# Kernel optimization log

Hardware: AMD Instinct MI355X
Metric: run time of the kernel (lower is better)

The kernel has to match this reference:

```python
import jax, jax.numpy as jnp
import numpy as np

N_NODES = 100000
N_EDGES = 1600000
D = 128  # feat_input_size_node == embed_inside_size == feat_target_size


def gcn_layer(x, W, b, row, col, ew, n_nodes):
    """PyG GCNConv with scalar edge_weight, add_self_loops=True, normalize=True.
    x: [N, Fin], W: [Fout, Fin], b: [Fout], row/col: [E], ew: [E].
    Messages flow row -> col (source_to_target)."""
    h = x @ W.T  # [N, Fout]
    # degree includes self-loop weight 1.0 per node
    deg = jax.ops.segment_sum(ew, col, num_segments=n_nodes) + 1.0  # [N]
    dinv = jnp.where(deg > 0, jax.lax.rsqrt(deg), 0.0)  # [N]
    norm = dinv[row] * ew * dinv[col]  # [E]
    msgs = norm[:, None] * h[row]  # [E, Fout] -- gather
    agg = jax.ops.segment_sum(msgs, col, num_segments=n_nodes)  # scatter-add
    agg = agg + (dinv * dinv)[:, None] * h  # self-loop contribution (weight 1)
    return agg + b


def setup_inputs() -> dict:
    key = jax.random.key(0)
    k1, k2, k3, k4, k5, k6, k7 = jax.random.split(key, 7)
    edge_tuples = jax.random.randint(k1, (2, N_EDGES), 0, N_NODES, dtype=jnp.int64) if jax.config.jax_enable_x64 else jax.random.randint(k1, (2, N_EDGES), 0, N_NODES).astype(jnp.int32)
    edge_feats = jax.random.uniform(k2, (N_EDGES, 1), dtype=jnp.float32)
    node_feats = jax.random.normal(k3, (N_NODES, D), dtype=jnp.float32)
    s1 = 1.0 / np.sqrt(D)
    W1 = jax.random.uniform(k4, (D, D), minval=-s1, maxval=s1, dtype=jnp.float32)
    b1 = jnp.zeros((D,), dtype=jnp.float32)
    W2 = jax.random.uniform(k5, (D, D), minval=-s1, maxval=s1, dtype=jnp.float32)
    b2 = jnp.zeros((D,), dtype=jnp.float32)
    return {"edge_tuples": edge_tuples, "edge_feats": edge_feats, "node_feats": node_feats,
            "W1": W1, "b1": b1, "W2": W2, "b2": b2}


def reference(edge_tuples, edge_feats, node_feats, W1, b1, W2, b2):
    row, col = edge_tuples[0], edge_tuples[1]
    ew = edge_feats.squeeze(-1)  # [E]
    n = node_feats.shape[0]
    h = gcn_layer(node_feats, W1, b1, row, col, ew, n)
    h = jnp.tanh(h)  # activate='tanh' between the two GCN layers
    out = gcn_layer(h, W2, b2, row, col, ew, n)
    # skip=Identity (Fin==Fout), doskip=1
    return out + node_feats
```

## Files before the change

### kernel.cpp

```cpp
#include <hip/hip_runtime.h>
#include <math.h>

#define D 128
#define SCAN_T 256
#define EPB 4096
#define MAXNB 800

typedef unsigned long long ull;
typedef unsigned short ushort_t;
typedef __attribute__((ext_vector_type(8))) short bf16x8;
typedef __attribute__((ext_vector_type(4))) float f32x4;

__device__ __forceinline__ float bf_lo(unsigned u) { return __uint_as_float(u << 16); }
__device__ __forceinline__ float bf_hi(unsigned u) { return __uint_as_float(u & 0xffff0000u); }
__device__ __forceinline__ unsigned bpack(float a, float b) {
  unsigned ua = __float_as_uint(a), ub = __float_as_uint(b);
  ua += 0x7fff + ((ua >> 16) & 1);
  ub += 0x7fff + ((ub >> 16) & 1);
  return (ua >> 16) | (ub & 0xffff0000u);
}
__device__ __forceinline__ ushort_t bh16(float a) {
  unsigned ua = __float_as_uint(a);
  ua += 0x7fff + ((ua >> 16) & 1);
  return (ushort_t)(ua >> 16);
}

__global__ __launch_bounds__(256) void k_h1(const int* __restrict__ col, int E, int B1, int B1pad,
                                            int* __restrict__ gh, int NB,
                                            const float2* __restrict__ x2, unsigned* __restrict__ xb, int n64,
                                            const float* __restrict__ W1, const float* __restrict__ W2,
                                            ushort_t* __restrict__ Whi1, ushort_t* __restrict__ Wlo1,
                                            ushort_t* __restrict__ Whi2, ushort_t* __restrict__ Wlo2) {
  int b = blockIdx.x, t = threadIdx.x;
  if (b < B1) {
    __shared__ int h[MAXNB];
    for (int i = t; i < NB; i += 256) h[i] = 0;
    __syncthreads();
    int e0 = b * EPB, e1 = min(E, e0 + EPB);
    for (int e = e0 + t; e < e1; e += 256) atomicAdd(&h[col[e] >> 7], 1);
    __syncthreads();
    for (int i = t; i < NB; i += 256) gh[i * B1pad + b] = h[i];
    return;
  }
  int idx = (b - B1) * 256 + t;
  if (idx < n64) { float2 v = x2[idx]; xb[idx] = bpack(v.x, v.y); return; }
  int j = idx - n64;
  if (j >= 2 * D * D) return;
  const float* W = (j < D * D) ? W1 : W2;
  ushort_t* Hh = (j < D * D) ? Whi1 : Whi2;
  ushort_t* Hl = (j < D * D) ? Wlo1 : Wlo2;
  int k = j & (D * D - 1);
  float w = W[k];
  ushort_t hh = bh16(w);
  Hh[k] = hh;
  Hl[k] = bh16(w - __uint_as_float((unsigned)hh << 16));
}

__global__ __launch_bounds__(512) void k_hscan(int* __restrict__ gh, int* __restrict__ binTotal,
                                               int B1, int B1pad) {
  __shared__ int wsum[8];
  int bin = blockIdx.x, t = threadIdx.x;
  int v = (t < B1) ? gh[bin * B1pad + t] : 0;
  int lane = t & 63, wid = t >> 6;
  int x = v;
  #pragma unroll
  for (int d = 1; d < 64; d <<= 1) { int y = __shfl_up(x, d, 64); if (lane >= d) x += y; }
  if (lane == 63) wsum[wid] = x;
  __syncthreads();
  int woff = 0;
  for (int w = 0; w < wid; ++w) woff += wsum[w];
  if (t < B1) gh[bin * B1pad + t] = woff + x - v;
  if (t == 511) binTotal[bin] = woff + x;
}

__device__ __forceinline__ int block_excl_scan(int v, int t, int* wsum, int* total) {
  int lane = t & 63, wid = t >> 6;
  int x = v;
  #pragma unroll
  for (int d = 1; d < 64; d <<= 1) {
    int y = __shfl_up(x, d, 64);
    if (lane >= d) x += y;
  }
  if (lane == 63) wsum[wid] = x;
  __syncthreads();
  int woff = 0;
  for (int w = 0; w < wid; ++w) woff += wsum[w];
  if (total) { int tot = 0; for (int w = 0; w < 4; ++w) tot += wsum[w]; *total = tot; }
  return woff + x - v;
}

__global__ __launch_bounds__(SCAN_T) void k_hscan2(const int* __restrict__ binTotal,
                                                   int* __restrict__ binBase,
                                                   int* __restrict__ offs, int NB, int N) {
  __shared__ int wsum[4];
  int t = threadIdx.x;
  int base = t * 4;
  int v[4]; int s = 0;
  #pragma unroll
  for (int u = 0; u < 4; ++u) { v[u] = (base + u < NB) ? binTotal[base + u] : 0; s += v[u]; }
  int tot;
  int excl = block_excl_scan(s, t, wsum, &tot);
  int run = excl;
  #pragma unroll
  for (int u = 0; u < 4; ++u) { if (base + u < NB) binBase[base + u] = run; run += v[u]; }
  if (t == 0) { binBase[NB] = tot; offs[N] = tot; }
}

__global__ __launch_bounds__(256) void k_scatter(const int* __restrict__ row, const int* __restrict__ col,
                                                 const float* __restrict__ ew,
                                                 const int* __restrict__ gh, const int* __restrict__ binBase,
                                                 int B1pad, int NB,
                                                 ull* __restrict__ a_e, int E) {
  __shared__ ull recs[EPB];
  __shared__ int hist[MAXNB];
  __shared__ int cur[MAXNB];
  __shared__ int wb[MAXNB];
  __shared__ int wsum[4];
  int b = blockIdx.x, t = threadIdx.x;
  for (int i = t; i < NB; i += 256) { hist[i] = 0; cur[i] = 0; }
  __syncthreads();
  int e0 = b * EPB;
  int cnt = min(E - e0, EPB);
  ull v[16];
  #pragma unroll
  for (int k = 0; k < 16; ++k) {
    int idx = t + k * 256;
    v[k] = 0;
    if (idx < cnt) {
      int e = e0 + idx;
      int c = col[e];
      unsigned q = __float2uint_rn(ew[e] * 32767.0f);
      if (q > 32767u) q = 32767u;
      unsigned hi = ((unsigned)c << 15) | q;
      v[k] = ((ull)hi << 32) | (unsigned)row[e];
      atomicAdd(&hist[hi >> 22], 1);
    }
  }
  __syncthreads();
  int base = t * 4;
  int hv[4];
  #pragma unroll
  for (int u = 0; u < 4; ++u) hv[u] = (base + u < NB) ? hist[base + u] : 0;
  int s = hv[0] + hv[1] + hv[2] + hv[3];
  int excl = block_excl_scan(s, t, wsum, nullptr);
  int run = excl;
  #pragma unroll
  for (int u = 0; u < 4; ++u) {
    if (base + u < NB) {
      hist[base + u] = run;
      wb[base + u] = binBase[base + u] + gh[(base + u) * B1pad + b] - run;
    }
    run += hv[u];
  }
  __syncthreads();
  #pragma unroll
  for (int k = 0; k < 16; ++k) {
    if (t + k * 256 < cnt) {
      unsigned bkt = (unsigned)(v[k] >> 54);
      int idx = hist[bkt] + atomicAdd(&cur[bkt], 1);
      recs[idx] = v[k];
    }
  }
  __syncthreads();
  for (int i = t; i < cnt; i += 256) {
    ull r = recs[i];
    a_e[wb[(unsigned)(r >> 54)] + i] = r;
  }
}

__global__ __launch_bounds__(256) void k_bucket(const ull* __restrict__ a_e,
                                                const int* __restrict__ binBase,
                                                int* __restrict__ offs, float* __restrict__ dinv,
                                                unsigned* __restrict__ sorted2, int N) {
  __shared__ int hist[128];
  __shared__ float wdeg[128];
  __shared__ int pfx[128];
  __shared__ int cur[128];
  int bin = blockIdx.x, t = threadIdx.x;
  if (t < 128) { hist[t] = 0; wdeg[t] = 0.f; cur[t] = 0; }
  __syncthreads();
  int s0 = binBase[bin], s1 = binBase[bin + 1];
  for (int i = s0 + t; i < s1; i += 256) {
    unsigned hi = (unsigned)(a_e[i] >> 32);
    int lc = (hi >> 15) & 127;
    atomicAdd(&hist[lc], 1);
    atomicAdd(&wdeg[lc], (float)(hi & 32767u) * (1.0f / 32767.0f));
  }
  __syncthreads();
  if (t == 0) { int run = 0; for (int i = 0; i < 128; ++i) { pfx[i] = run; run += hist[i]; } }
  __syncthreads();
  int c0 = bin << 7;
  if (t < 128 && c0 + t < N) {
    offs[c0 + t] = s0 + pfx[t];
    dinv[c0 + t] = rsqrtf(wdeg[t] + 1.0f);
  }
  for (int i = s0 + t; i < s1; i += 256) {
    ull v = a_e[i];
    unsigned hi = (unsigned)(v >> 32);
    int lc = (hi >> 15) & 127;
    int pos = s0 + pfx[lc] + atomicAdd(&cur[lc], 1);
    sorted2[pos] = ((unsigned)v << 15) | (hi & 32767u);
  }
}

__global__ void k_norm(unsigned* __restrict__ el, const int* __restrict__ offs,
                       const float* __restrict__ dinv, int N) {
  int c = blockIdx.x * blockDim.x + threadIdx.x;
  if (c >= N) return;
  int s0 = offs[c], s1 = offs[c + 1];
  float dc = dinv[c] * (1.0f / 32767.0f);
  for (int i = s0; i < s1; ++i) {
    unsigned v = el[i];
    unsigned r = v >> 15;
    float nrm = dinv[r] * (float)(v & 32767u) * dc;
    unsigned q = __float2uint_rn(nrm * 32767.0f);
    if (q > 32767u) q = 32767u;
    el[i] = (r << 15) | q;
  }
}

__global__ __launch_bounds__(256) void k_agg(const unsigned* __restrict__ H2,
                                             const unsigned* __restrict__ elist,
                                             const int* __restrict__ offs, const float* __restrict__ dinv,
                                             unsigned* __restrict__ outb, int N) {
  int lane = threadIdx.x & 63;
  int c = blockIdx.x * 4 + (threadIdx.x >> 6);
  if (c >= N) return;
  int start = offs[c];
  int m = offs[c + 1] - start;
  int q = lane >> 4;
  int fi = lane & 15;
  float a0 = 0.f, a1 = 0.f, a2 = 0.f, a3 = 0.f, a4 = 0.f, a5 = 0.f, a6 = 0.f, a7 = 0.f;
  for (int base = 0; base < m; base += 64) {
    int chunk = min(64, m - base);
    unsigned rec = (lane < chunk) ? elist[start + base + lane] : 0u;
    int iters = (chunk + 3) >> 2;
    int i = 0;
    for (; i + 4 <= iters; i += 4) {
      unsigned e0 = __shfl(rec, 4 * i + q, 64);
      unsigned e1 = __shfl(rec, 4 * i + 4 + q, 64);
      unsigned e2 = __shfl(rec, 4 * i + 8 + q, 64);
      unsigned e3 = __shfl(rec, 4 * i + 12 + q, 64);
      uint4 u0 = *(const uint4*)&H2[(size_t)(e0 >> 15) * 64 + fi * 4];
      uint4 u1 = *(const uint4*)&H2[(size_t)(e1 >> 15) * 64 + fi * 4];
      uint4 u2 = *(const uint4*)&H2[(size_t)(e2 >> 15) * 64 + fi * 4];
      uint4 u3 = *(const uint4*)&H2[(size_t)(e3 >> 15) * 64 + fi * 4];
      float w0 = (float)(e0 & 0x7fffu) * (1.0f / 32767.0f);
      float w1 = (float)(e1 & 0x7fffu) * (1.0f / 32767.0f);
      float w2 = (float)(e2 & 0x7fffu) * (1.0f / 32767.0f);
      float w3 = (float)(e3 & 0x7fffu) * (1.0f / 32767.0f);
      a0 += w0 * bf_lo(u0.x); a1 += w0 * bf_hi(u0.x);
      a2 += w0 * bf_lo(u0.y); a3 += w0 * bf_hi(u0.y);
      a4 += w0 * bf_lo(u0.z); a5 += w0 * bf_hi(u0.z);
      a6 += w0 * bf_lo(u0.w); a7 += w0 * bf_hi(u0.w);
      a0 += w1 * bf_lo(u1.x); a1 += w1 * bf_hi(u1.x);
      a2 += w1 * bf_lo(u1.y); a3 += w1 * bf_hi(u1.y);
      a4 += w1 * bf_lo(u1.z); a5 += w1 * bf_hi(u1.z);
      a6 += w1 * bf_lo(u1.w); a7 += w1 * bf_hi(u1.w);
      a0 += w2 * bf_lo(u2.x); a1 += w2 * bf_hi(u2.x);
      a2 += w2 * bf_lo(u2.y); a3 += w2 * bf_hi(u2.y);
      a4 += w2 * bf_lo(u2.z); a5 += w2 * bf_hi(u2.z);
      a6 += w2 * bf_lo(u2.w); a7 += w2 * bf_hi(u2.w);
      a0 += w3 * bf_lo(u3.x); a1 += w3 * bf_hi(u3.x);
      a2 += w3 * bf_lo(u3.y); a3 += w3 * bf_hi(u3.y);
      a4 += w3 * bf_lo(u3.z); a5 += w3 * bf_hi(u3.z);
      a6 += w3 * bf_lo(u3.w); a7 += w3 * bf_hi(u3.w);
    }
    for (; i < iters; ++i) {
      unsigned e0 = __shfl(rec, 4 * i + q, 64);
      float w0 = (float)(e0 & 0x7fffu) * (1.0f / 32767.0f);
      uint4 u0 = *(const uint4*)&H2[(size_t)(e0 >> 15) * 64 + fi * 4];
      a0 += w0 * bf_lo(u0.x); a1 += w0 * bf_hi(u0.x);
      a2 += w0 * bf_lo(u0.y); a3 += w0 * bf_hi(u0.y);
      a4 += w0 * bf_lo(u0.z); a5 += w0 * bf_hi(u0.z);
      a6 += w0 * bf_lo(u0.w); a7 += w0 * bf_hi(u0.w);
    }
  }
  a0 += __shfl_xor(a0, 16, 64); a0 += __shfl_xor(a0, 32, 64);
  a1 += __shfl_xor(a1, 16, 64); a1 += __shfl_xor(a1, 32, 64);
  a2 += __shfl_xor(a2, 16, 64); a2 += __shfl_xor(a2, 32, 64);
  a3 += __shfl_xor(a3, 16, 64); a3 += __shfl_xor(a3, 32, 64);
  a4 += __shfl_xor(a4, 16, 64); a4 += __shfl_xor(a4, 32, 64);
  a5 += __shfl_xor(a5, 16, 64); a5 += __shfl_xor(a5, 32, 64);
  a6 += __shfl_xor(a6, 16, 64); a6 += __shfl_xor(a6, 32, 64);
  a7 += __shfl_xor(a7, 16, 64); a7 += __shfl_xor(a7, 32, 64);
  if (q == 0) {
    float dv = dinv[c], sw = dv * dv;
    uint4 us = *(const uint4*)&H2[(size_t)c * 64 + fi * 4];
    a0 += sw * bf_lo(us.x); a1 += sw * bf_hi(us.x);
    a2 += sw * bf_lo(us.y); a3 += sw * bf_hi(us.y);
    a4 += sw * bf_lo(us.z); a5 += sw * bf_hi(us.z);
    a6 += sw * bf_lo(us.w); a7 += sw * bf_hi(us.w);
    uint4 o;
    o.x = bpack(a0, a1); o.y = bpack(a2, a3); o.z = bpack(a4, a5); o.w = bpack(a6, a7);
    *(uint4*)&outb[(size_t)c * 64 + fi * 4] = o;
  }
}

template<int TANH, int SKIP>
__global__ __launch_bounds__(256) void k_mgemm(const ushort_t* __restrict__ S,
                                               const ushort_t* __restrict__ Whi,
                                               const ushort_t* __restrict__ Wlo,
                                               const float* __restrict__ bias,
                                               const ushort_t* __restrict__ skipb,
                                               void* __restrict__ outv, int n) {
  int wave = threadIdx.x >> 6, lane = threadIdx.x & 63;
  int cl = lane & 15;
  int kg = lane >> 4;
  int cb0 = wave * 2;

  bf16x8 bh[2][4], bl[2][4];
  float bv[2];
  #pragma unroll
  for (int c = 0; c < 2; ++c) {
    int col = (cb0 + c) * 16 + cl;
    const ushort_t* wh = Whi + (size_t)col * D + kg * 8;
    const ushort_t* wl = Wlo + (size_t)col * D + kg * 8;
    #pragma unroll
    for (int kt = 0; kt < 4; ++kt) {
      bh[c][kt] = *(const bf16x8*)(wh + kt * 32);
      bl[c][kt] = *(const bf16x8*)(wl + kt * 32);
    }
    bv[c] = bias[col];
  }

  int ntiles = (n + 15) >> 4;
  for (int t = blockIdx.x; t < ntiles; t += gridDim.x) {
    int arow = t * 16 + cl; if (arow >= n) arow = n - 1;
    const ushort_t* srow = S + (size_t)arow * D + kg * 8;
    bf16x8 a[4];
    #pragma unroll
    for (int kt = 0; kt < 4; ++kt) a[kt] = *(const bf16x8*)(srow + kt * 32);
    #pragma unroll
    for (int c = 0; c < 2; ++c) {
      f32x4 acc = {0.f, 0.f, 0.f, 0.f};
      #pragma unroll
      for (int kt = 0; kt < 4; ++kt)
        acc = __builtin_amdgcn_mfma_f32_16x16x32_bf16(a[kt], bh[c][kt], acc, 0, 0, 0);
      #pragma unroll
      for (int kt = 0; kt < 4; ++kt)
        acc = __builtin_amdgcn_mfma_f32_16x16x32_bf16(a[kt], bl[c][kt], acc, 0, 0, 0);
      int col = (cb0 + c) * 16 + cl;
      #pragma unroll
      for (int i = 0; i < 4; ++i) {
        int r = t * 16 + kg * 4 + i;
        if (r < n) {
          float o = acc[i] + bv[c];
          if (TANH) {
            o = tanhf(o);
            ((ushort_t*)outv)[(size_t)r * D + col] = bh16(o);
          } else {
            if (SKIP) o += __uint_as_float((unsigned)skipb[(size_t)r * D + col] << 16);
            ((float*)outv)[(size_t)r * D + col] = o;
          }
        }
      }
    }
  }
}

extern "C" void kernel_launch(void* const* d_in, const int* in_sizes, int n_in,
                              void* d_out, int out_size, void* d_ws, size_t ws_size,
                              hipStream_t stream) {
  const int*   et = (const int*)d_in[0];
  const float* ef = (const float*)d_in[1];
  const float* x  = (const float*)d_in[2];
  const float* W1 = (const float*)d_in[3];
  const float* b1 = (const float*)d_in[4];
  const float* W2 = (const float*)d_in[5];
  const float* b2 = (const float*)d_in[6];

  int E = in_sizes[1];
  int N = in_sizes[2] / D;
  const int* row = et;
  const int* col = et + E;

  int NB = (N + 127) >> 7;
  int B1 = (E + EPB - 1) / EPB;
  int B1pad = (B1 + 7) & ~7;

  char* p = (char*)d_ws;
  auto alloc = [&](size_t bytes) { char* q = p; p += (bytes + 255) & ~(size_t)255; return q; };
  int*      gh       = (int*)     alloc((size_t)NB * B1pad * 4);
  int*      binTotal = (int*)     alloc((size_t)NB * 4);
  int*      binBase  = (int*)     alloc((size_t)(NB + 1) * 4);
  ull*      a_e      = (ull*)     alloc((size_t)E * 8);
  unsigned* elist    = (unsigned*)alloc((size_t)E * 4);
  int*      offs     = (int*)     alloc((size_t)(N + 1) * 4);
  float*    dinv     = (float*)   alloc((size_t)N * 4);
  unsigned* xb       = (unsigned*)alloc((size_t)N * 64 * 4);
  unsigned* s2b      = (unsigned*)alloc((size_t)N * 64 * 4);
  ushort_t* whi1 = (ushort_t*)alloc(D * D * 2);
  ushort_t* wlo1 = (ushort_t*)alloc(D * D * 2);
  ushort_t* whi2 = (ushort_t*)alloc(D * D * 2);
  ushort_t* wlo2 = (ushort_t*)alloc(D * D * 2);
  unsigned* s1b = (unsigned*)d_out;
  unsigned* a1b = s1b + (size_t)N * 64;

  int prepBlocks = (N * 64 + 2 * D * D + 255) / 256;
  k_h1<<<B1 + prepBlocks, 256, 0, stream>>>(col, E, B1, B1pad, gh, NB,
                                            (const float2*)x, xb, N * 64,
                                            W1, W2, whi1, wlo1, whi2, wlo2);
  k_hscan<<<NB, 512, 0, stream>>>(gh, binTotal, B1, B1pad);
  k_hscan2<<<1, SCAN_T, 0, stream>>>(binTotal, binBase, offs, NB, N);
  k_scatter<<<B1, 256, 0, stream>>>(row, col, ef, gh, binBase, B1pad, NB, a_e, E);
  k_bucket<<<NB, 256, 0, stream>>>(a_e, binBase, offs, dinv, elist, N);
  k_norm<<<(N + 255) / 256, 256, 0, stream>>>(elist, offs, dinv, N);

  int ab = (N + 3) / 4;
  int gb = 1024;
  k_agg<<<ab, 256, 0, stream>>>(xb, elist, offs, dinv, s1b, N);
  k_mgemm<1, 0><<<gb, 256, 0, stream>>>((const ushort_t*)s1b, whi1, wlo1, b1, nullptr, a1b, N);
  k_agg<<<ab, 256, 0, stream>>>(a1b, elist, offs, dinv, s2b, N);
  k_mgemm<0, 1><<<gb, 256, 0, stream>>>((const ushort_t*)s2b, whi2, wlo2, b2,
                                        (const ushort_t*)xb, d_out, N);
}
```

Measured before the change: 256.7 us.

## Fold bin scan into scatter/bucket kernels and compute edge norm inside aggregation

Removes the single-block bin-prefix-scan kernel: k_scatter now redoes the exclusive scan of binTotal in every block, and k_bucket computes its own start offset with a block reduction. It also drops the k_norm pass over the edge list, so k_agg multiplies the raw quantized edge weight by dinv[row] and dinv[col] on the fly. This saves two launches and one read-modify-write pass over the edge list. In exchange each gathered edge needs an extra random dinv load in both aggregation passes, and the scan work is repeated redundantly in every block.

```diff
diff --git a/kernel.cpp b/kernel.cpp
--- a/kernel.cpp
+++ b/kernel.cpp
@@ -2,7 +2,6 @@
 #include <math.h>
 
 #define D 128
-#define SCAN_T 256
 #define EPB 4096
 #define MAXNB 800
 
@@ -89,32 +88,16 @@
   return woff + x - v;
 }
 
-__global__ __launch_bounds__(SCAN_T) void k_hscan2(const int* __restrict__ binTotal,
-                                                   int* __restrict__ binBase,
-                                                   int* __restrict__ offs, int NB, int N) {
-  __shared__ int wsum[4];
-  int t = threadIdx.x;
-  int base = t * 4;
-  int v[4]; int s = 0;
-  #pragma unroll
-  for (int u = 0; u < 4; ++u) { v[u] = (base + u < NB) ? binTotal[base + u] : 0; s += v[u]; }
-  int tot;
-  int excl = block_excl_scan(s, t, wsum, &tot);
-  int run = excl;
-  #pragma unroll
-  for (int u = 0; u < 4; ++u) { if (base + u < NB) binBase[base + u] = run; run += v[u]; }
-  if (t == 0) { binBase[NB] = tot; offs[N] = tot; }
-}
-
 __global__ __launch_bounds__(256) void k_scatter(const int* __restrict__ row, const int* __restrict__ col,
                                                  const float* __restrict__ ew,
-                                                 const int* __restrict__ gh, const int* __restrict__ binBase,
+                                                 const int* __restrict__ gh, const int* __restrict__ binTotal,
                                                  int B1pad, int NB,
                                                  ull* __restrict__ a_e, int E) {
   __shared__ ull recs[EPB];
   __shared__ int hist[MAXNB];
   __shared__ int cur[MAXNB];
   __shared__ int wb[MAXNB];
+  __shared__ int bbase[MAXNB];
   __shared__ int wsum[4];
   int b = blockIdx.x, t = threadIdx.x;
   for (int i = t; i < NB; i += 256) { hist[i] = 0; cur[i] = 0; }
@@ -138,6 +121,16 @@
   }
   __syncthreads();
   int base = t * 4;
+  int bt[4]; int sb = 0;
+  #pragma unroll
+  for (int u = 0; u < 4; ++u) { bt[u] = (base + u < NB) ? binTotal[base + u] : 0; sb += bt[u]; }
+  int exb = block_excl_scan(sb, t, wsum, nullptr);
+  {
+    int run = exb;
+    #pragma unroll
+    for (int u = 0; u < 4; ++u) { if (base + u < NB) bbase[base + u] = run; run += bt[u]; }
+  }
+  __syncthreads();
   int hv[4];
   #pragma unroll
   for (int u = 0; u < 4; ++u) hv[u] = (base + u < NB) ? hist[base + u] : 0;
@@ -148,7 +141,7 @@
   for (int u = 0; u < 4; ++u) {
     if (base + u < NB) {
       hist[base + u] = run;
-      wb[base + u] = binBase[base + u] + gh[(base + u) * B1pad + b] - run;
+      wb[base + u] = bbase[base + u] + gh[(base + u) * B1pad + b] - run;
     }
     run += hv[u];
   }
@@ -169,17 +162,28 @@
 }
 
 __global__ __launch_bounds__(256) void k_bucket(const ull* __restrict__ a_e,
-                                                const int* __restrict__ binBase,
+                                                const int* __restrict__ binTotal,
                                                 int* __restrict__ offs, float* __restrict__ dinv,
-                                                unsigned* __restrict__ sorted2, int N) {
+                                                unsigned* __restrict__ sorted2, int N, int E, int NB) {
   __shared__ int hist[128];
   __shared__ float wdeg[128];
   __shared__ int pfx[128];
   __shared__ int cur[128];
+  __shared__ int wred[4];
+  __shared__ int s0sh;
   int bin = blockIdx.x, t = threadIdx.x;
   if (t < 128) { hist[t] = 0; wdeg[t] = 0.f; cur[t] = 0; }
-  __syncthreads();
-  int s0 = binBase[bin], s1 = binBase[bin + 1];
+  int part = 0;
+  for (int j = t; j < NB; j += 256) if (j < bin) part += binTotal[j];
+  #pragma unroll
+  for (int d = 32; d >= 1; d >>= 1) part += __shfl_xor(part, d, 64);
+  if ((t & 63) == 0) wred[t >> 6] = part;
+  __syncthreads();
+  if (t == 0) s0sh = wred[0] + wred[1] + wred[2] + wred[3];
+  if (t == 0 && bin == 0) offs[N] = E;
+  __syncthreads();
+  int s0 = s0sh;
+  int s1 = s0 + binTotal[bin];
   for (int i = s0 + t; i < s1; i += 256) {
     unsigned hi = (unsigned)(a_e[i] >> 32);
     int lc = (hi >> 15) & 127;
@@ -200,22 +204,6 @@
     int lc = (hi >> 15) & 127;
     int pos = s0 + pfx[lc] + atomicAdd(&cur[lc], 1);
     sorted2[pos] = ((unsigned)v << 15) | (hi & 32767u);
-  }
-}
-
-__global__ void k_norm(unsigned* __restrict__ el, const int* __restrict__ offs,
-                       const float* __restrict__ dinv, int N) {
-  int c = blockIdx.x * blockDim.x + threadIdx.x;
-  if (c >= N) return;
-  int s0 = offs[c], s1 = offs[c + 1];
-  float dc = dinv[c] * (1.0f / 32767.0f);
-  for (int i = s0; i < s1; ++i) {
-    unsigned v = el[i];
-    unsigned r = v >> 15;
-    float nrm = dinv[r] * (float)(v & 32767u) * dc;
-    unsigned q = __float2uint_rn(nrm * 32767.0f);
-    if (q > 32767u) q = 32767u;
-    el[i] = (r << 15) | q;
   }
 }
 
@@ -230,6 +218,8 @@
   int m = offs[c + 1] - start;
   int q = lane >> 4;
   int fi = lane & 15;
+  float dv = dinv[c];
+  float dcs = dv * (1.0f / 32767.0f);
   float a0 = 0.f, a1 = 0.f, a2 = 0.f, a3 = 0.f, a4 = 0.f, a5 = 0.f, a6 = 0.f, a7 = 0.f;
   for (int base = 0; base < m; base += 64) {
     int chunk = min(64, m - base);
@@ -245,10 +235,10 @@
       uint4 u1 = *(const uint4*)&H2[(size_t)(e1 >> 15) * 64 + fi * 4];
       uint4 u2 = *(const uint4*)&H2[(size_t)(e2 >> 15) * 64 + fi * 4];
       uint4 u3 = *(const uint4*)&H2[(size_t)(e3 >> 15) * 64 + fi * 4];
-      float w0 = (float)(e0 & 0x7fffu) * (1.0f / 32767.0f);
-      float w1 = (float)(e1 & 0x7fffu) * (1.0f / 32767.0f);
-      float w2 = (float)(e2 & 0x7fffu) * (1.0f / 32767.0f);
-      float w3 = (float)(e3 & 0x7fffu) * (1.0f / 32767.0f);
+      float w0 = (float)(e0 & 0x7fffu) * dinv[e0 >> 15] * dcs;
+      float w1 = (float)(e1 & 0x7fffu) * dinv[e1 >> 15] * dcs;
+      float w2 = (float)(e2 & 0x7fffu) * dinv[e2 >> 15] * dcs;
+      float w3 = (float)(e3 & 0x7fffu) * dinv[e3 >> 15] * dcs;
       a0 += w0 * bf_lo(u0.x); a1 += w0 * bf_hi(u0.x);
       a2 += w0 * bf_lo(u0.y); a3 += w0 * bf_hi(u0.y);
       a4 += w0 * bf_lo(u0.z); a5 += w0 * bf_hi(u0.z);
@@ -268,7 +258,7 @@
     }
     for (; i < iters; ++i) {
       unsigned e0 = __shfl(rec, 4 * i + q, 64);
-      float w0 = (float)(e0 & 0x7fffu) * (1.0f / 32767.0f);
+      float w0 = (float)(e0 & 0x7fffu) * dinv[e0 >> 15] * dcs;
       uint4 u0 = *(const uint4*)&H2[(size_t)(e0 >> 15) * 64 + fi * 4];
       a0 += w0 * bf_lo(u0.x); a1 += w0 * bf_hi(u0.x);
       a2 += w0 * bf_lo(u0.y); a3 += w0 * bf_hi(u0.y);
@@ -285,7 +275,7 @@
   a6 += __shfl_xor(a6, 16, 64); a6 += __shfl_xor(a6, 32, 64);
   a7 += __shfl_xor(a7, 16, 64); a7 += __shfl_xor(a7, 32, 64);
   if (q == 0) {
-    float dv = dinv[c], sw = dv * dv;
+    float sw = dv * dv;
     uint4 us = *(const uint4*)&H2[(size_t)c * 64 + fi * 4];
     a0 += sw * bf_lo(us.x); a1 += sw * bf_hi(us.x);
     a2 += sw * bf_lo(us.y); a3 += sw * bf_hi(us.y);
@@ -383,7 +373,6 @@
   auto alloc = [&](size_t bytes) { char* q = p; p += (bytes + 255) & ~(size_t)255; return q; };
   int*      gh       = (int*)     alloc((size_t)NB * B1pad * 4);
   int*      binTotal = (int*)     alloc((size_t)NB * 4);
-  int*      binBase  = (int*)     alloc((size_t)(NB + 1) * 4);
   ull*      a_e      = (ull*)     alloc((size_t)E * 8);
   unsigned* elist    = (unsigned*)alloc((size_t)E * 4);
   int*      offs     = (int*)     alloc((size_t)(N + 1) * 4);
@@ -402,10 +391,8 @@
                                             (const float2*)x, xb, N * 64,
                                             W1, W2, whi1, wlo1, whi2, wlo2);
   k_hscan<<<NB, 512, 0, stream>>>(gh, binTotal, B1, B1pad);
-  k_hscan2<<<1, SCAN_T, 0, stream>>>(binTotal, binBase, offs, NB, N);
-  k_scatter<<<B1, 256, 0, stream>>>(row, col, ef, gh, binBase, B1pad, NB, a_e, E);
-  k_bucket<<<NB, 256, 0, stream>>>(a_e, binBase, offs, dinv, elist, N);
-  k_norm<<<(N + 255) / 256, 256, 0, stream>>>(elist, offs, dinv, N);
+  k_scatter<<<B1, 256, 0, stream>>>(row, col, ef, gh, binTotal, B1pad, NB, a_e, E);
+  k_bucket<<<NB, 256, 0, stream>>>(a_e, binTotal, offs, dinv, elist, N, E, NB);
 
   int ab = (N + 3) / 4;
   int gb = 1024;
```

Result: faster. 240.0 us (-6.5%).
